# Performance work log

Hardware: AMD Instinct MI355X
Metric: run time of the kernel (lower is better)

## Reference

```python
import jax, jax.numpy as jnp
import numpy as np

N_NODES = 50000
N_EDGES = 800000
D = 64
L = 3


def setup_inputs() -> dict:
    key = jax.random.key(0)
    ks = jax.random.split(key, 6)
    glorot = (6.0 / (D + D)) ** 0.5  # xavier_uniform bound for [D,D]
    return {
        "x": jax.random.normal(ks[0], (N_NODES, D), dtype=jnp.float32),
        "edge_index": jax.random.randint(ks[1], (2, N_EDGES), 0, N_NODES, dtype=jnp.int32),
        "edge_weight": jax.random.uniform(ks[2], (N_EDGES,), dtype=jnp.float32),
        "W_rel": jax.random.uniform(ks[3], (L, D, D), jnp.float32, -glorot, glorot),
        "b_rel": jnp.zeros((L, D), dtype=jnp.float32),
        "W_root": jax.random.uniform(ks[4], (L, D, D), jnp.float32, -glorot, glorot),
    }


def reference(x, edge_index, edge_weight, W_rel, b_rel, W_root):
    """myGNN_hidden.full_forward final embedding: L GraphConv(add) layers, tanh on last.
    GraphConv: h_i' = h_i @ W_root + (sum_{j->i} e_ji * h_j) @ W_rel + b_rel.
    """
    src, dst = edge_index[0], edge_index[1]
    n = x.shape[0]
    h = x
    num_layers = W_rel.shape[0]
    for i in range(num_layers):
        msg = edge_weight[:, None] * h[src]                      # [E, D] gather + scale
        agg = jax.ops.segment_sum(msg, dst, num_segments=n)      # [N, D] scatter-add
        h = agg @ W_rel[i] + b_rel[i] + h @ W_root[i]
        if i == num_layers - 1:
            h = jnp.tanh(h)
    return h
```

## Files before the change

kernel.cpp:

```cpp
#include <hip/hip_runtime.h>
#include <hip/hip_bf16.h>

#define NN 50000
#define NE 800000
#define DD 64
#define NL 3
#define NE_PAD (NE + NN * 16)

__device__ __forceinline__ float rlane(float v, int l) {
    return __int_as_float(__builtin_amdgcn_readlane(__float_as_int(v), l));
}

__global__ void hist_kernel(const int* __restrict__ dst,
                            int* __restrict__ deg,
                            int* __restrict__ rank) {
    int t = blockIdx.x * blockDim.x + threadIdx.x;
    int e = t * 4;
    if (e + 4 <= NE) {
        int4 d4 = *reinterpret_cast<const int4*>(dst + e);
        int r0 = atomicAdd(&deg[d4.x], 1);
        int r1 = atomicAdd(&deg[d4.y], 1);
        int r2 = atomicAdd(&deg[d4.z], 1);
        int r3 = atomicAdd(&deg[d4.w], 1);
        *reinterpret_cast<int4*>(rank + e) = make_int4(r0, r1, r2, r3);
    } else {
        for (int i = e; i < NE; ++i) rank[i] = atomicAdd(&deg[dst[i]], 1);
    }
}

__global__ void alloc_kernel(const int* __restrict__ deg,
                             int* __restrict__ row_start,
                             int* __restrict__ counter) {
    int n = blockIdx.x * blockDim.x + threadIdx.x;
    int lane = threadIdx.x & 63;
    int d = (n < NN) ? ((deg[n] + 15) & ~15) : 0;
    int s = d;
    #pragma unroll
    for (int off = 1; off < 64; off <<= 1) {
        int t = __shfl_up(s, off);
        if (lane >= off) s += t;
    }
    int total = __shfl(s, 63);
    int base = 0;
    if (lane == 63) base = atomicAdd(counter, total);
    base = __shfl(base, 63);
    int my = base + s - d;
    if (n < NN) row_start[n] = my;
}

__global__ void reorder_kernel(const int* __restrict__ src,
                               const int* __restrict__ dst,
                               const float* __restrict__ w,
                               const int* __restrict__ rank,
                               const int* __restrict__ row_start,
                               int2* __restrict__ e_sw) {
    int t = blockIdx.x * blockDim.x + threadIdx.x;
    int e = t * 2;
    if (e + 2 <= NE) {
        int2   s2 = *reinterpret_cast<const int2*>(src + e);
        int2   d2 = *reinterpret_cast<const int2*>(dst + e);
        float2 w2 = *reinterpret_cast<const float2*>(w + e);
        int2   r2 = *reinterpret_cast<const int2*>(rank + e);
        e_sw[row_start[d2.x] + r2.x] = make_int2(s2.x, __float_as_int(w2.x));
        e_sw[row_start[d2.y] + r2.y] = make_int2(s2.y, __float_as_int(w2.y));
    } else {
        for (int i = e; i < NE; ++i) {
            e_sw[row_start[dst[i]] + rank[i]] = make_int2(src[i], __float_as_int(w[i]));
        }
    }
}

__global__ void __launch_bounds__(256, 8)
gather_kernel(const float* __restrict__ h,
              const int* __restrict__ row_start,
              const int* __restrict__ deg,
              const int2* __restrict__ e_sw,
              float* __restrict__ agg) {
    int wid = __builtin_amdgcn_readfirstlane((int)((blockIdx.x * blockDim.x + threadIdx.x) >> 6));
    if (wid >= NN) return;
    const int lane = threadIdx.x & 63;
    const int g    = lane >> 4;
    const int cq   = (lane & 15) << 2;
    const int beg  = __builtin_amdgcn_readfirstlane(row_start[wid]);
    const int rdeg = __builtin_amdgcn_readfirstlane((deg[wid] + 15) & ~15);

    float ax0=0.f, ay0=0.f, az0=0.f, aw0=0.f;
    float ax1=0.f, ay1=0.f, az1=0.f, aw1=0.f;
    float ax2=0.f, ay2=0.f, az2=0.f, aw2=0.f;
    float ax3=0.f, ay3=0.f, az3=0.f, aw3=0.f;

    for (int i = 0; i < rdeg; i += 16) {
        const int2* ep = e_sw + beg + i;
        int2 m0 = ep[0],  m1 = ep[1],  m2 = ep[2],  m3 = ep[3];
        int2 m4 = ep[4],  m5 = ep[5],  m6 = ep[6],  m7 = ep[7];
        int2 m8 = ep[8],  m9 = ep[9],  m10= ep[10], m11= ep[11];
        int2 m12= ep[12], m13= ep[13], m14= ep[14], m15= ep[15];

#define SLOT(AX,AY,AZ,AW, EA,EB,EC,ED)                                          \
        {                                                                       \
            int  srcg = (g==0) ? EA.x : (g==1) ? EB.x : (g==2) ? EC.x : ED.x;   \
            int  wig  = (g==0) ? EA.y : (g==1) ? EB.y : (g==2) ? EC.y : ED.y;   \
            float wg  = __int_as_float(wig);                                    \
            const float4 r = *reinterpret_cast<const float4*>(                  \
                h + (size_t)srcg * DD + cq);                                    \
            AX += wg * r.x; AY += wg * r.y; AZ += wg * r.z; AW += wg * r.w;     \
        }
        SLOT(ax0,ay0,az0,aw0, m0,m1,m2,m3)
        SLOT(ax1,ay1,az1,aw1, m4,m5,m6,m7)
        SLOT(ax2,ay2,az2,aw2, m8,m9,m10,m11)
        SLOT(ax3,ay3,az3,aw3, m12,m13,m14,m15)
#undef SLOT
    }

    float tx = (ax0+ax1)+(ax2+ax3);
    float ty = (ay0+ay1)+(ay2+ay3);
    float tz = (az0+az1)+(az2+az3);
    float tw = (aw0+aw1)+(aw2+aw3);
    tx += __shfl_xor(tx, 16); tx += __shfl_xor(tx, 32);
    ty += __shfl_xor(ty, 16); ty += __shfl_xor(ty, 32);
    tz += __shfl_xor(tz, 16); tz += __shfl_xor(tz, 32);
    tw += __shfl_xor(tw, 16); tw += __shfl_xor(tw, 32);

    if (lane < 16) {
        float4 t = make_float4(tx, ty, tz, tw);
        *reinterpret_cast<float4*>(agg + (size_t)wid * DD + cq) = t;
    }
}

template<bool LAST>
__global__ void __launch_bounds__(256, 3)
dense_kernel(const float* __restrict__ agg,
             const float* h,
             const float* __restrict__ Wrel,
             const float* __restrict__ Wroot,
             const float* __restrict__ b,
             float* hout) {
    const int lane   = threadIdx.x & 63;
    const int wgid   = __builtin_amdgcn_readfirstlane((int)((blockIdx.x * blockDim.x + threadIdx.x) >> 6));
    const int nwaves = (gridDim.x * blockDim.x) >> 6;

    float w1[DD], w2[DD];
    #pragma unroll
    for (int k = 0; k < DD; ++k) {
        w1[k] = Wrel[k * DD + lane];
        w2[k] = Wroot[k * DD + lane];
    }
    const float bias = b[lane];

    for (int n = wgid; n < NN; n += nwaves) {
        const float vagg = agg[(size_t)n * DD + lane];
        const float vh   = h[(size_t)n * DD + lane];
        float a0 = bias, a1 = 0.f, a2 = 0.f, a3 = 0.f;
        #pragma unroll
        for (int k = 0; k < DD; k += 2) {
            float sa0 = rlane(vagg, k),     sh0 = rlane(vh, k);
            float sa1 = rlane(vagg, k + 1), sh1 = rlane(vh, k + 1);
            a0 += sa0 * w1[k];
            a1 += sh0 * w2[k];
            a2 += sa1 * w1[k + 1];
            a3 += sh1 * w2[k + 1];
        }
        float r = (a0 + a1) + (a2 + a3);
        if (LAST) r = tanhf(r);
        hout[(size_t)n * DD + lane] = r;
    }
}

extern "C" void kernel_launch(void* const* d_in, const int* in_sizes, int n_in,
                              void* d_out, int out_size, void* d_ws, size_t ws_size,
                              hipStream_t stream) {
    const float* x     = (const float*)d_in[0];
    const int*   ei    = (const int*)d_in[1];
    const float* ew    = (const float*)d_in[2];
    const float* Wrel  = (const float*)d_in[3];
    const float* brel  = (const float*)d_in[4];
    const float* Wroot = (const float*)d_in[5];
    float* out = (float*)d_out;

    float* agg       = (float*)d_ws;
    float* hA        = agg + (size_t)NN * DD;
    int2*  e_sw      = (int2*)(hA + (size_t)NN * DD);
    int*   row_start = (int*)(e_sw + NE_PAD);
    int*   deg       = row_start + NN;
    int*   counter   = deg + NN;
    int*   rank      = counter + 1;

    const int* src = ei;
    const int* dst = ei + NE;

    const int hblocks = (NE / 4 + 255) / 256;
    const int rblocks = (NE / 2 + 255) / 256;
    const int ablocks = (NN + 255) / 256;
    const int gblocks = (NN * 64 + 255) / 256;
    const int dblocks = 1024;

    hipMemsetAsync(deg, 0, (size_t)(NN + 1) * sizeof(int), stream);
    hipMemsetAsync(e_sw, 0, (size_t)NE_PAD * sizeof(int2), stream);
    hist_kernel<<<hblocks, 256, 0, stream>>>(dst, deg, rank);
    alloc_kernel<<<ablocks, 256, 0, stream>>>(deg, row_start, counter);
    reorder_kernel<<<rblocks, 256, 0, stream>>>(src, dst, ew, rank, row_start, e_sw);

    gather_kernel<<<gblocks, 256, 0, stream>>>(x, row_start, deg, e_sw, agg);
    dense_kernel<false><<<dblocks, 256, 0, stream>>>(agg, x, Wrel, Wroot, brel, hA);
    gather_kernel<<<gblocks, 256, 0, stream>>>(hA, row_start, deg, e_sw, agg);
    dense_kernel<false><<<dblocks, 256, 0, stream>>>(agg, hA, Wrel + DD*DD, Wroot + DD*DD, brel + DD, hA);
    gather_kernel<<<gblocks, 256, 0, stream>>>(hA, row_start, deg, e_sw, agg);
    dense_kernel<true ><<<dblocks, 256, 0, stream>>>(agg, hA, Wrel + 2*DD*DD, Wroot + 2*DD*DD, brel + 2*DD, out);
}
```

Baseline: 302.6 us.

## Fuse gather and dense transform into one per-layer kernel with ping-pong buffers

Merges the per-node neighbor gather and the two 64x64 matvecs into a single kernel per layer, so the aggregated row stays in registers instead of being written to and re-read from global memory. The fused kernel loads weights from global/L1 per k inside the node loop rather than caching them in registers. The row is read back through readlane on the distributed float4 layout. Uses separate hA/hB buffers and merges the two memsets into one by placing deg and counter right after e_sw. This cuts three kernel launches and the agg round trip, at the cost of repeated weight loads and a persistent-grid loop that may balance irregular degrees less well.

```diff
diff --git a/kernel.cpp b/kernel.cpp
--- a/kernel.cpp
+++ b/kernel.cpp
@@ -70,96 +70,76 @@
     }
 }
 
-__global__ void __launch_bounds__(256, 8)
-gather_kernel(const float* __restrict__ h,
-              const int* __restrict__ row_start,
-              const int* __restrict__ deg,
-              const int2* __restrict__ e_sw,
-              float* __restrict__ agg) {
-    int wid = __builtin_amdgcn_readfirstlane((int)((blockIdx.x * blockDim.x + threadIdx.x) >> 6));
-    if (wid >= NN) return;
+template<bool LAST>
+__global__ void __launch_bounds__(256, 3)
+fused_kernel(const float* __restrict__ h,
+             const int* __restrict__ row_start,
+             const int* __restrict__ deg,
+             const int2* __restrict__ e_sw,
+             const float* __restrict__ Wrel,
+             const float* __restrict__ Wroot,
+             const float* __restrict__ b,
+             float* __restrict__ hout) {
     const int lane = threadIdx.x & 63;
     const int g    = lane >> 4;
     const int cq   = (lane & 15) << 2;
-    const int beg  = __builtin_amdgcn_readfirstlane(row_start[wid]);
-    const int rdeg = __builtin_amdgcn_readfirstlane((deg[wid] + 15) & ~15);
-
-    float ax0=0.f, ay0=0.f, az0=0.f, aw0=0.f;
-    float ax1=0.f, ay1=0.f, az1=0.f, aw1=0.f;
-    float ax2=0.f, ay2=0.f, az2=0.f, aw2=0.f;
-    float ax3=0.f, ay3=0.f, az3=0.f, aw3=0.f;
-
-    for (int i = 0; i < rdeg; i += 16) {
-        const int2* ep = e_sw + beg + i;
-        int2 m0 = ep[0],  m1 = ep[1],  m2 = ep[2],  m3 = ep[3];
-        int2 m4 = ep[4],  m5 = ep[5],  m6 = ep[6],  m7 = ep[7];
-        int2 m8 = ep[8],  m9 = ep[9],  m10= ep[10], m11= ep[11];
-        int2 m12= ep[12], m13= ep[13], m14= ep[14], m15= ep[15];
-
-#define SLOT(AX,AY,AZ,AW, EA,EB,EC,ED)                                          \
-        {                                                                       \
-            int  srcg = (g==0) ? EA.x : (g==1) ? EB.x : (g==2) ? EC.x : ED.x;   \
-            int  wig  = (g==0) ? EA.y : (g==1) ? EB.y : (g==2) ? EC.y : ED.y;   \
-            float wg  = __int_as_float(wig);                                    \
-            const float4 r = *reinterpret_cast<const float4*>(                  \
-                h + (size_t)srcg * DD + cq);                                    \
-            AX += wg * r.x; AY += wg * r.y; AZ += wg * r.z; AW += wg * r.w;     \
-        }
-        SLOT(ax0,ay0,az0,aw0, m0,m1,m2,m3)
-        SLOT(ax1,ay1,az1,aw1, m4,m5,m6,m7)
-        SLOT(ax2,ay2,az2,aw2, m8,m9,m10,m11)
-        SLOT(ax3,ay3,az3,aw3, m12,m13,m14,m15)
-#undef SLOT
-    }
-
-    float tx = (ax0+ax1)+(ax2+ax3);
-    float ty = (ay0+ay1)+(ay2+ay3);
-    float tz = (az0+az1)+(az2+az3);
-    float tw = (aw0+aw1)+(aw2+aw3);
-    tx += __shfl_xor(tx, 16); tx += __shfl_xor(tx, 32);
-    ty += __shfl_xor(ty, 16); ty += __shfl_xor(ty, 32);
-    tz += __shfl_xor(tz, 16); tz += __shfl_xor(tz, 32);
-    tw += __shfl_xor(tw, 16); tw += __shfl_xor(tw, 32);
-
-    if (lane < 16) {
-        float4 t = make_float4(tx, ty, tz, tw);
-        *reinterpret_cast<float4*>(agg + (size_t)wid * DD + cq) = t;
-    }
-}
-
-template<bool LAST>
-__global__ void __launch_bounds__(256, 3)
-dense_kernel(const float* __restrict__ agg,
-             const float* h,
-             const float* __restrict__ Wrel,
-             const float* __restrict__ Wroot,
-             const float* __restrict__ b,
-             float* hout) {
-    const int lane   = threadIdx.x & 63;
-    const int wgid   = __builtin_amdgcn_readfirstlane((int)((blockIdx.x * blockDim.x + threadIdx.x) >> 6));
-    const int nwaves = (gridDim.x * blockDim.x) >> 6;
-
-    float w1[DD], w2[DD];
-    #pragma unroll
-    for (int k = 0; k < DD; ++k) {
-        w1[k] = Wrel[k * DD + lane];
-        w2[k] = Wroot[k * DD + lane];
-    }
+    const int wid0 = (int)((blockIdx.x * blockDim.x + threadIdx.x) >> 6);
+    const int nw   = (gridDim.x * blockDim.x) >> 6;
     const float bias = b[lane];
 
-    for (int n = wgid; n < NN; n += nwaves) {
-        const float vagg = agg[(size_t)n * DD + lane];
-        const float vh   = h[(size_t)n * DD + lane];
+    for (int nn = wid0; nn < NN; nn += nw) {
+        const int n    = __builtin_amdgcn_readfirstlane(nn);
+        const int beg  = __builtin_amdgcn_readfirstlane(row_start[n]);
+        const int rdeg = __builtin_amdgcn_readfirstlane((deg[n] + 15) & ~15);
+
+        float ax0=0.f, ay0=0.f, az0=0.f, aw0=0.f;
+        float ax1=0.f, ay1=0.f, az1=0.f, aw1=0.f;
+        float ax2=0.f, ay2=0.f, az2=0.f, aw2=0.f;
+        float ax3=0.f, ay3=0.f, az3=0.f, aw3=0.f;
+        for (int i = 0; i < rdeg; i += 16) {
+            const int2* ep = e_sw + beg + i;
+            int2 m0 = ep[0],  m1 = ep[1],  m2 = ep[2],  m3 = ep[3];
+            int2 m4 = ep[4],  m5 = ep[5],  m6 = ep[6],  m7 = ep[7];
+            int2 m8 = ep[8],  m9 = ep[9],  m10= ep[10], m11= ep[11];
+            int2 m12= ep[12], m13= ep[13], m14= ep[14], m15= ep[15];
+#define SLOT(AX,AY,AZ,AW, EA,EB,EC,ED)                                          \
+            {                                                                   \
+                int  srcg = (g==0) ? EA.x : (g==1) ? EB.x : (g==2) ? EC.x : ED.x;\
+                int  wig  = (g==0) ? EA.y : (g==1) ? EB.y : (g==2) ? EC.y : ED.y;\
+                float wg  = __int_as_float(wig);                                \
+                const float4 r = *reinterpret_cast<const float4*>(              \
+                    h + (size_t)srcg * DD + cq);                                \
+                AX += wg * r.x; AY += wg * r.y; AZ += wg * r.z; AW += wg * r.w; \
+            }
+            SLOT(ax0,ay0,az0,aw0, m0,m1,m2,m3)
+            SLOT(ax1,ay1,az1,aw1, m4,m5,m6,m7)
+            SLOT(ax2,ay2,az2,aw2, m8,m9,m10,m11)
+            SLOT(ax3,ay3,az3,aw3, m12,m13,m14,m15)
+#undef SLOT
+        }
+        float tx = (ax0+ax1)+(ax2+ax3);
+        float ty = (ay0+ay1)+(ay2+ay3);
+        float tz = (az0+az1)+(az2+az3);
+        float tw = (aw0+aw1)+(aw2+aw3);
+        tx += __shfl_xor(tx, 16); tx += __shfl_xor(tx, 32);
+        ty += __shfl_xor(ty, 16); ty += __shfl_xor(ty, 32);
+        tz += __shfl_xor(tz, 16); tz += __shfl_xor(tz, 32);
+        tw += __shfl_xor(tw, 16); tw += __shfl_xor(tw, 32);
+
+        const float4 hv = *reinterpret_cast<const float4*>(h + (size_t)n * DD + cq);
+
         float a0 = bias, a1 = 0.f, a2 = 0.f, a3 = 0.f;
+#define DK(K, ACC, TC, HC)                                                      \
+        ACC += rlane(TC, (K) >> 2) * Wrel[(K) * DD + lane]                      \
+             + rlane(HC, (K) >> 2) * Wroot[(K) * DD + lane];
         #pragma unroll
-        for (int k = 0; k < DD; k += 2) {
-            float sa0 = rlane(vagg, k),     sh0 = rlane(vh, k);
-            float sa1 = rlane(vagg, k + 1), sh1 = rlane(vh, k + 1);
-            a0 += sa0 * w1[k];
-            a1 += sh0 * w2[k];
-            a2 += sa1 * w1[k + 1];
-            a3 += sh1 * w2[k + 1];
+        for (int k = 0; k < DD; k += 4) {
+            DK(k + 0, a0, tx, hv.x)
+            DK(k + 1, a1, ty, hv.y)
+            DK(k + 2, a2, tz, hv.z)
+            DK(k + 3, a3, tw, hv.w)
         }
+#undef DK
         float r = (a0 + a1) + (a2 + a3);
         if (LAST) r = tanhf(r);
         hout[(size_t)n * DD + lane] = r;
@@ -177,13 +157,13 @@
     const float* Wroot = (const float*)d_in[5];
     float* out = (float*)d_out;
 
-    float* agg       = (float*)d_ws;
-    float* hA        = agg + (size_t)NN * DD;
-    int2*  e_sw      = (int2*)(hA + (size_t)NN * DD);
-    int*   row_start = (int*)(e_sw + NE_PAD);
-    int*   deg       = row_start + NN;
+    float* hA        = (float*)d_ws;
+    float* hB        = hA + (size_t)NN * DD;
+    int2*  e_sw      = (int2*)(hB + (size_t)NN * DD);
+    int*   deg       = (int*)(e_sw + NE_PAD);
     int*   counter   = deg + NN;
-    int*   rank      = counter + 1;
+    int*   row_start = counter + 1;
+    int*   rank      = row_start + NN;
 
     const int* src = ei;
     const int* dst = ei + NE;
@@ -191,19 +171,14 @@
     const int hblocks = (NE / 4 + 255) / 256;
     const int rblocks = (NE / 2 + 255) / 256;
     const int ablocks = (NN + 255) / 256;
-    const int gblocks = (NN * 64 + 255) / 256;
-    const int dblocks = 1024;
+    const int fblocks = 1563;
 
-    hipMemsetAsync(deg, 0, (size_t)(NN + 1) * sizeof(int), stream);
-    hipMemsetAsync(e_sw, 0, (size_t)NE_PAD * sizeof(int2), stream);
+    hipMemsetAsync(e_sw, 0, (size_t)NE_PAD * sizeof(int2) + (size_t)(NN + 1) * sizeof(int), stream);
     hist_kernel<<<hblocks, 256, 0, stream>>>(dst, deg, rank);
     alloc_kernel<<<ablocks, 256, 0, stream>>>(deg, row_start, counter);
     reorder_kernel<<<rblocks, 256, 0, stream>>>(src, dst, ew, rank, row_start, e_sw);
 
-    gather_kernel<<<gblocks, 256, 0, stream>>>(x, row_start, deg, e_sw, agg);
-    dense_kernel<false><<<dblocks, 256, 0, stream>>>(agg, x, Wrel, Wroot, brel, hA);
-    gather_kernel<<<gblocks, 256, 0, stream>>>(hA, row_start, deg, e_sw, agg);
-    dense_kernel<false><<<dblocks, 256, 0, stream>>>(agg, hA, Wrel + DD*DD, Wroot + DD*DD, brel + DD, hA);
-    gather_kernel<<<gblocks, 256, 0, stream>>>(hA, row_start, deg, e_sw, agg);
-    dense_kernel<true ><<<dblocks, 256, 0, stream>>>(agg, hA, Wrel + 2*DD*DD, Wroot + 2*DD*DD, brel + 2*DD, out);
+    fused_kernel<false><<<fblocks, 256, 0, stream>>>(x,  row_start, deg, e_sw, Wrel,           Wroot,           brel,        hA);
+    fused_kernel<false><<<fblocks, 256, 0, stream>>>(hA, row_start, deg, e_sw, Wrel + DD*DD,   Wroot + DD*DD,   brel + DD,   hB);
+    fused_kernel<true ><<<fblocks, 256, 0, stream>>>(hB, row_start, deg, e_sw, Wrel + 2*DD*DD, Wroot + 2*DD*DD, brel + 2*DD, out);
 }
```

Result: slower. 380.7 us (+25.8%).
